# Performance work log

Measured on AMD Instinct MI355X. Metric: run time of the kernel, lower is better.

## Reference

```python
import jax, jax.numpy as jnp
import numpy as np

B, S, T, E, H, V = 32, 64, 64, 512, 512, 32000  # batch, src len, tgt len, embed, hidden(per dir), vocab


def _lstm_scan(xs, Wih, Whh, bih, bhh, h0, c0):
    # xs: [S, B, E]; PyTorch gate order i, f, g, o
    def step(carry, x):
        h, c = carry
        g = x @ Wih.T + bih + h @ Whh.T + bhh
        i, f, gg, o = jnp.split(g, 4, axis=-1)
        c = jax.nn.sigmoid(f) * c + jax.nn.sigmoid(i) * jnp.tanh(gg)
        h = jax.nn.sigmoid(o) * jnp.tanh(c)
        return (h, c), h
    (hT, cT), hs = jax.lax.scan(step, (h0, c0), xs)
    return hs, hT, cT


def setup_inputs() -> dict:
    key = jax.random.key(0)
    ks = jax.random.split(key, 20)
    p = lambda k, shape, s=0.05: (jax.random.normal(k, shape, jnp.float32) * s)
    inp = {
        "input_chunk": jax.random.randint(ks[0], (B, S), 0, V),
        "target_chunk": jax.random.randint(ks[1], (B, T), 0, V),
        "enc_emb": jax.random.uniform(ks[2], (V, E), jnp.float32, -0.1, 0.1),
        "dec_emb": jax.random.uniform(ks[3], (V, E), jnp.float32, -0.1, 0.1),
        # encoder bidirectional LSTM (1 layer)
        "Wih_f": p(ks[4], (4 * H, E)), "Whh_f": p(ks[5], (4 * H, H)),
        "bih_f": p(ks[6], (4 * H,)), "bhh_f": p(ks[7], (4 * H,)),
        "Wih_b": p(ks[8], (4 * H, E)), "Whh_b": p(ks[9], (4 * H, H)),
        "bih_b": p(ks[10], (4 * H,)), "bhh_b": p(ks[11], (4 * H,)),
        # decoder LSTMCell: input 2H+E, hidden 2H
        "Wih_d": p(ks[12], (8 * H, 2 * H + E)), "Whh_d": p(ks[13], (8 * H, 2 * H)),
        "bih_d": p(ks[14], (8 * H,)), "bhh_d": p(ks[15], (8 * H,)),
        # attention projection 2H -> 2H
        "Wa": p(ks[16], (2 * H, 2 * H)), "ba": p(ks[17], (2 * H,)),
        # output projection 2H -> V (bias initialized to 0 in the module)
        "Wout": p(ks[18], (V, 2 * H)), "bout": jnp.zeros((V,), jnp.float32),
    }
    return inp


def reference(input_chunk, target_chunk, enc_emb, dec_emb,
              Wih_f, Whh_f, bih_f, bhh_f, Wih_b, Whh_b, bih_b, bhh_b,
              Wih_d, Whh_d, bih_d, bhh_d, Wa, ba, Wout, bout):
    # ---- Encoder: bidirectional LSTM ----
    x = enc_emb[input_chunk]                 # [B, S, E]
    xs = jnp.transpose(x, (1, 0, 2))         # [S, B, E]
    h0 = jnp.zeros((B, H), x.dtype)
    c0 = jnp.zeros((B, H), x.dtype)
    hs_f, hT_f, cT_f = _lstm_scan(xs, Wih_f, Whh_f, bih_f, bhh_f, h0, c0)
    hs_b, hT_b, cT_b = _lstm_scan(xs[::-1], Wih_b, Whh_b, bih_b, bhh_b, h0, c0)
    hs_b = hs_b[::-1]
    all_hidden = jnp.concatenate([hs_f, hs_b], axis=-1)          # [S, B, 2H]
    all_hidden = jnp.transpose(all_hidden, (1, 0, 2))            # [B, S, 2H]
    dec_h = jnp.concatenate([hT_f, hT_b], axis=-1)               # [B, 2H]
    dec_c = jnp.concatenate([cT_f, cT_b], axis=-1)               # [B, 2H]

    # ---- Decoder: attention + LSTMCell loop (teacher forcing = 1.0, no dropout) ----
    A = all_hidden @ Wa.T + ba               # W_attention(all_hidden), constant across steps
    tgt_emb = dec_emb[target_chunk]          # [B, T, E]
    # feed at t=0 is zeros; afterwards the t-th target embedding
    feeds = jnp.concatenate([jnp.zeros((B, 1, E), tgt_emb.dtype), tgt_emb[:, :-1]], axis=1)
    feeds = jnp.transpose(feeds, (1, 0, 2))  # [T, B, E]

    def dstep(carry, feed):
        h, c = carry
        scores = jnp.einsum('bsd,bd->bs', A, h)                  # [B, S]
        attn = jax.nn.softmax(scores, axis=1)
        ctx = jnp.einsum('bs,bsd->bd', attn, all_hidden)         # [B, 2H]
        inp = jnp.concatenate([ctx, feed], axis=1)               # [B, 2H+E]
        g = inp @ Wih_d.T + bih_d + h @ Whh_d.T + bhh_d
        i, f, gg, o = jnp.split(g, 4, axis=-1)
        c = jax.nn.sigmoid(f) * c + jax.nn.sigmoid(i) * jnp.tanh(gg)
        h = jax.nn.sigmoid(o) * jnp.tanh(c)
        logits = h @ Wout.T + bout                               # [B, V]
        return (h, c), logits

    _, logits = jax.lax.scan(dstep, (dec_h, dec_c), feeds)       # [T, B, V]
    logits = jnp.transpose(logits, (1, 0, 2))                    # [B, T, V]
    outputs = jnp.argmax(logits, axis=-1)                        # [B, T]
    return logits, outputs
```

## Files before the change

kernel.cpp:

```cpp
#include <hip/hip_runtime.h>
#include <hip/hip_bf16.h>

#define BB 32
#define SS 64
#define TT 64
#define EE 512
#define HH 512
#define VV 32000

#define O_C0    0u
#define O_C1    32768u
#define O_HD    65536u
#define O_CD    98304u
#define O_PENC  131072u
#define O_PDEC  655360u
#define O_CTX   1179648u
#define O_ALLH  1212416u
#define O_AATT  3309568u
#define O_HDEC  5406720u
#define O_PACK  7503872u
#define O_DA1   7507968u
#define O_DA2   7540736u
#define O_W1    7573504u
#define WS_NEED 95830016ull

#define S_GXF   0u
#define S_GXB   4194304u
#define S_GFEED 8388608u
#define U_BASE  17000000u

typedef float f32x4 __attribute__((ext_vector_type(4)));
typedef _Float16 f16x8 __attribute__((ext_vector_type(8)));
typedef _Float16 f16x4 __attribute__((ext_vector_type(4)));

__device__ __forceinline__ float sigm_(float x){ return 1.0f/(1.0f + expf(-x)); }

__device__ __forceinline__ unsigned int fkey_(float f){
  unsigned int u = __float_as_uint(f);
  return (u & 0x80000000u) ? ~u : (u | 0x80000000u);
}

__device__ __forceinline__ int swz_(int row, int kb){
  return (row*64 + kb) ^ ((row & 7) << 4);
}

__global__ __launch_bounds__(256) void k_init(float* __restrict__ ws){
  int i = blockIdx.x*256 + threadIdx.x;
  if (i < 65536) ws[i] = 0.0f;
  if (i < 2048) ((unsigned long long*)(ws + O_PACK))[i] = 0ull;
}

__global__ __launch_bounds__(256) void k_cvtW(
    const float* __restrict__ Whh_f, const float* __restrict__ Whh_b,
    const float* __restrict__ Wih_d, const float* __restrict__ Whh_d,
    _Float16* __restrict__ dst)
{
  int g = blockIdx.x*256 + threadIdx.x;
  int idx = g*4;
  f32x4 v;
  if (idx < 1048576){
    v = *(const f32x4*)(Whh_f + idx);
  } else if (idx < 2097152){
    v = *(const f32x4*)(Whh_b + (idx - 1048576));
  } else {
    int j = idx - 2097152;
    int row = j >> 11, col = j & 2047;
    const float* src = (col < 1024) ? (Wih_d + (size_t)row*1536 + col)
                                    : (Whh_d + (size_t)row*1024 + (col - 1024));
    v = *(const f32x4*)src;
  }
  f16x4 h;
  #pragma unroll
  for (int c = 0; c < 4; ++c) h[c] = (_Float16)v[c];
  *(f16x4*)(dst + idx) = h;
}

__global__ __launch_bounds__(256) void k_cvtWout(
    const float* __restrict__ Wout, _Float16* __restrict__ W1)
{
  size_t i = ((size_t)blockIdx.x*256 + threadIdx.x)*8;
  f32x4 x0 = *(const f32x4*)(Wout + i);
  f32x4 x1 = *(const f32x4*)(Wout + i + 4);
  f16x4 h0, h1;
  #pragma unroll
  for (int c = 0; c < 4; ++c){ h0[c] = (_Float16)x0[c]; h1[c] = (_Float16)x1[c]; }
  *(f16x4*)(W1 + i)   = h0;
  *(f16x4*)(W1 + i+4) = h1;
}

template<int MODE>
__global__ __launch_bounds__(256) void k_gemm(
    const float* __restrict__ A, int lda,
    const int* __restrict__ chunk,
    const float* __restrict__ W, int ldW,
    const float* __restrict__ bias0, const float* __restrict__ bias1,
    float* __restrict__ C, int ldC, int K)
{
  __shared__ float As[16*68];
  __shared__ float Bs[16*68];
  int tid = threadIdx.x;
  int n0 = blockIdx.x*64, m0 = blockIdx.y*64;
  int tx = tid & 15, ty = tid >> 4;
  int lrow = tid >> 2, kq = tid & 3;

  const float* arp;
  if (MODE == 0) {
    arp = A + (size_t)(m0 + lrow)*lda;
  } else if (MODE == 1) {
    int m = m0 + lrow; int s = m >> 5, b = m & 31;
    arp = A + (size_t)chunk[b*SS + s]*EE;
  } else {
    int m = m0 + lrow; int t = m >> 5, b = m & 31;
    arp = (t == 0) ? nullptr : A + (size_t)chunk[b*TT + (t-1)]*EE;
  }
  const float* wrp = W + (size_t)(n0 + lrow)*ldW;

  float acc[4][4] = {};
  for (int k0 = 0; k0 < K; k0 += 16){
    float4 va = make_float4(0.f,0.f,0.f,0.f);
    if (MODE == 0) va = *(const float4*)&arp[k0 + kq*4];
    else if (arp)  va = *(const float4*)&arp[k0 + kq*4];
    float4 vw = *(const float4*)&wrp[k0 + kq*4];
    As[(kq*4+0)*68 + lrow] = va.x;
    As[(kq*4+1)*68 + lrow] = va.y;
    As[(kq*4+2)*68 + lrow] = va.z;
    As[(kq*4+3)*68 + lrow] = va.w;
    Bs[(kq*4+0)*68 + lrow] = vw.x;
    Bs[(kq*4+1)*68 + lrow] = vw.y;
    Bs[(kq*4+2)*68 + lrow] = vw.z;
    Bs[(kq*4+3)*68 + lrow] = vw.w;
    __syncthreads();
    #pragma unroll
    for (int kk = 0; kk < 16; ++kk){
      float4 a4 = *(const float4*)&As[kk*68 + ty*4];
      float4 b4 = *(const float4*)&Bs[kk*68 + tx*4];
      float av[4] = {a4.x,a4.y,a4.z,a4.w};
      float bv[4] = {b4.x,b4.y,b4.z,b4.w};
      #pragma unroll
      for (int i=0;i<4;++i)
        #pragma unroll
        for (int j=0;j<4;++j)
          acc[i][j] = fmaf(av[i], bv[j], acc[i][j]);
    }
    __syncthreads();
  }
  float bv[4];
  #pragma unroll
  for (int j = 0; j < 4; ++j){
    int n = n0 + tx*4 + j;
    float bb = 0.f;
    if (bias0) bb += bias0[n];
    if (bias1) bb += bias1[n];
    bv[j] = bb;
  }
  #pragma unroll
  for (int i = 0; i < 4; ++i){
    int m = m0 + ty*4 + i;
    float4 v = make_float4(acc[i][0]+bv[0], acc[i][1]+bv[1], acc[i][2]+bv[2], acc[i][3]+bv[3]);
    *(float4*)&C[(size_t)m*ldC + n0 + tx*4] = v;
  }
}

__global__ __launch_bounds__(256) void k_enc_step(
    const _Float16* __restrict__ wenc,
    float* __restrict__ ws, const float* __restrict__ oscr, int t)
{
  __shared__ float hl[128*36];
  __shared__ float Wt[32*132];
  int sub = blockIdx.x, kp = blockIdx.y, dir = blockIdx.z;
  int tid = threadIdx.x;
  int s = dir ? (63 - t) : t;
  int p = t & 1;
  const float* gx  = oscr + (dir ? S_GXB : S_GXF);
  const float* prd = ws + (p ? O_PDEC : O_PENC) + dir*262144u;
  const float* cin = ws + O_C0 + p*32768u + dir*16384u;
  float* cout = ws + O_C0 + (p^1)*32768u + dir*16384u;

  {
    int ug = tid & 31, bg = tid >> 5;
    int ul0 = ug*4;
    int u0 = kp*128 + ul0;
    #pragma unroll
    for (int j = 0; j < 4; ++j){
      int b = bg*4 + j;
      size_t gbase = (size_t)(s*32 + b)*2048u;
      f32x4 g0 = *(const f32x4*)&gx[gbase + u0];
      f32x4 g1 = *(const f32x4*)&gx[gbase + 512 + u0];
      f32x4 g2 = *(const f32x4*)&gx[gbase + 1024 + u0];
      f32x4 g3 = *(const f32x4*)&gx[gbase + 1536 + u0];
      if (t > 0){
        #pragma unroll
        for (int kq = 0; kq < 4; ++kq){
          const float* pp = prd + kq*65536u + (size_t)b*2048u;
          g0 += *(const f32x4*)&pp[u0];
          g1 += *(const f32x4*)&pp[512 + u0];
          g2 += *(const f32x4*)&pp[1024 + u0];
          g3 += *(const f32x4*)&pp[1536 + u0];
        }
      }
      f32x4 c = *(const f32x4*)&cin[b*512 + u0];
      f32x4 cn, hn;
      #pragma unroll
      for (int e = 0; e < 4; ++e){
        float cc = sigm_(g1[e])*c[e] + sigm_(g0[e])*tanhf(g2[e]);
        float hh = sigm_(g3[e])*tanhf(cc);
        cn[e] = cc; hn[e] = hh;
        hl[(ul0+e)*36 + b] = hh;
      }
      if (sub == 0){
        *(f32x4*)&cout[b*512 + u0] = cn;
        *(f32x4*)&ws[O_ALLH + (size_t)(b*64 + s)*1024u + dir*512 + u0] = hn;
      }
    }
  }
  __syncthreads();
  if (t == 63) return;

  const _Float16* W = wenc + dir*1048576u;
  float* P = ws + (p ? O_PENC : O_PDEC) + dir*262144u + kp*65536u;
  int rg2 = tid & 31, bg2 = tid >> 5;
  int wrow = tid & 127, whalf = tid >> 7;
  float acc[4][4] = {};
  for (int kt = 0; kt < 4; ++kt){
    #pragma unroll
    for (int i = 0; i < 4; ++i){
      int chunk = whalf*4 + i;
      int grow = sub*128 + wrow;
      f16x4 v = *(const f16x4*)&W[(size_t)grow*512 + kp*128 + kt*32 + chunk*4];
      Wt[(chunk*4+0)*132 + wrow] = (float)v[0];
      Wt[(chunk*4+1)*132 + wrow] = (float)v[1];
      Wt[(chunk*4+2)*132 + wrow] = (float)v[2];
      Wt[(chunk*4+3)*132 + wrow] = (float)v[3];
    }
    __syncthreads();
    #pragma unroll 8
    for (int kk = 0; kk < 32; ++kk){
      f32x4 wv = *(const f32x4*)&Wt[kk*132 + rg2*4];
      f32x4 hv = *(const f32x4*)&hl[(kt*32+kk)*36 + bg2*4];
      #pragma unroll
      for (int i = 0; i < 4; ++i)
        #pragma unroll
        for (int j = 0; j < 4; ++j)
          acc[i][j] = fmaf(wv[i], hv[j], acc[i][j]);
    }
    __syncthreads();
  }
  #pragma unroll
  for (int j = 0; j < 4; ++j){
    int b = bg2*4 + j;
    f32x4 v; v[0]=acc[0][j]; v[1]=acc[1][j]; v[2]=acc[2][j]; v[3]=acc[3][j];
    *(f32x4*)&P[(size_t)b*2048u + sub*128 + rg2*4] = v;
  }
}

__global__ __launch_bounds__(256) void k_concat(float* __restrict__ ws){
  int i = blockIdx.x*256 + threadIdx.x;
  int which = i >> 15;
  int idx = i & 32767;
  int b = idx >> 10, u = idx & 1023;
  int dir = (u >= 512);
  int uu = u & 511;
  float v;
  if (which == 0){
    int s = dir ? 0 : 63;
    v = ws[O_ALLH + (size_t)(b*64 + s)*1024u + u];
  } else {
    v = ws[O_C0 + dir*16384u + b*512 + uu];
  }
  ws[(which ? O_CD : O_HD) + b*1024 + u] = v;
}

__global__ __launch_bounds__(256) void k_dec_gemm(
    const _Float16* __restrict__ wdec, float* __restrict__ ws)
{
  __shared__ char lds[16384];
  int nb = blockIdx.x, kp = blockIdx.y;
  int tid = threadIdx.x;
  int lane = tid & 63, w = tid >> 6;
  int lr = lane & 15, lg = lane >> 4;
  const _Float16* A1g = (const _Float16*)(ws + O_DA1);
  const _Float16* A2g = (const _Float16*)(ws + O_DA2);

  int aslot = tid & 127;
  int isA2  = tid >> 7;
  int arow = aslot >> 2, aseg = aslot & 3;
  int wrow = tid >> 2, wseg = tid & 3;
  const _Float16* asrc = (isA2 ? A2g : A1g) + (size_t)arow*2048u + kp*512 + aseg*8;
  const _Float16* wsrc = wdec + (size_t)(nb*64 + wrow)*2048u + kp*512 + wseg*8;

  f32x4 accH[2], accM[2];
  #pragma unroll
  for (int i = 0; i < 2; ++i){ f32x4 z; z[0]=z[1]=z[2]=z[3]=0.f; accH[i]=z; accM[i]=z; }

  uint4 rA = *(const uint4*)(asrc);
  uint4 rW = *(const uint4*)(wsrc);

  for (int kt = 0; kt < 16; ++kt){
    int cur = kt & 1;
    char* base = lds + cur*8192;
    *(uint4*)(base + (isA2 ? 2048 : 0) + swz_(arow, aseg*16)) = rA;
    *(uint4*)(base + 4096 + swz_(wrow, wseg*16)) = rW;
    __syncthreads();
    if (kt < 15){
      rA = *(const uint4*)(asrc + (kt+1)*32);
      rW = *(const uint4*)(wsrc + (kt+1)*32);
    }
    char* A1t = base, *A2t = base + 2048, *Wt = base + 4096;
    f16x8 wf = *(const f16x8*)(Wt + swz_(w*16 + lr, lg*16));
    #pragma unroll
    for (int mf = 0; mf < 2; ++mf){
      f16x8 a1 = *(const f16x8*)(A1t + swz_(mf*16 + lr, lg*16));
      f16x8 a2 = *(const f16x8*)(A2t + swz_(mf*16 + lr, lg*16));
      accH[mf] = __builtin_amdgcn_mfma_f32_16x16x32_f16(a1, wf, accH[mf], 0, 0, 0);
      accM[mf] = __builtin_amdgcn_mfma_f32_16x16x32_f16(a2, wf, accM[mf], 0, 0, 0);
    }
    __syncthreads();
  }
  const float rs = 1.0f/2048.0f;
  float* P = ws + O_PDEC + (size_t)kp*131072u;
  #pragma unroll
  for (int mf = 0; mf < 2; ++mf)
    #pragma unroll
    for (int r = 0; r < 4; ++r){
      int b = mf*16 + lg*4 + r;
      int n = nb*64 + w*16 + lr;
      P[(size_t)b*4096u + n] = accH[mf][r] + accM[mf][r]*rs;
    }
}

__global__ __launch_bounds__(256) void k_attn(float* __restrict__ ws,
                                              const float* __restrict__ oscr, int t){
  __shared__ float hlq[1024];
  __shared__ float part[64][5];
  __shared__ float sc[64];
  __shared__ float atn[64];
  __shared__ float dsh;
  int b = blockIdx.x, tid = threadIdx.x;
  float* hd = ws + O_HD;
  float* cd = ws + O_CD;
  _Float16* DA1 = (_Float16*)(ws + O_DA1);
  _Float16* DA2 = (_Float16*)(ws + O_DA2);
  if (t > 0){
    const float* gfd = oscr + S_GFEED + (size_t)((t-1)*32 + b)*4096u;
    const float* pd = ws + O_PDEC;
    for (int u = tid; u < 1024; u += 256){
      float g0 = gfd[u], g1 = gfd[1024+u], g2 = gfd[2048+u], g3 = gfd[3072+u];
      #pragma unroll
      for (int kp = 0; kp < 4; ++kp){
        const float* p = pd + (size_t)kp*131072u + (size_t)b*4096u;
        g0 += p[u]; g1 += p[1024+u]; g2 += p[2048+u]; g3 += p[3072+u];
      }
      float c = cd[b*1024 + u];
      c = sigm_(g1)*c + sigm_(g0)*tanhf(g2);
      float h = sigm_(g3)*tanhf(c);
      cd[b*1024+u] = c; hd[b*1024+u] = h; hlq[u] = h;
      ws[O_HDEC + (size_t)(b*64 + (t-1))*1024u + u] = h;
      _Float16 hi = (_Float16)h;
      DA1[(size_t)b*2048u + 1024 + u] = hi;
      DA2[(size_t)b*2048u + 1024 + u] = (_Float16)((h - (float)hi)*2048.0f);
    }
  } else {
    for (int u = tid; u < 1024; u += 256){
      float h = hd[b*1024 + u];
      hlq[u] = h;
      _Float16 hi = (_Float16)h;
      DA1[(size_t)b*2048u + 1024 + u] = hi;
      DA2[(size_t)b*2048u + 1024 + u] = (_Float16)((h - (float)hi)*2048.0f);
    }
  }
  __syncthreads();
  {
    int s = tid >> 2, p = tid & 3;
    const float* Ar = ws + O_AATT + (size_t)(b*64 + s)*1024u + p*256;
    const float* hp = &hlq[p*256];
    float sum = 0.f;
    #pragma unroll 8
    for (int k4 = 0; k4 < 64; ++k4){
      float4 a = *(const float4*)&Ar[k4*4];
      float4 h4 = *(const float4*)&hp[k4*4];
      sum = fmaf(a.x,h4.x, fmaf(a.y,h4.y, fmaf(a.z,h4.z, fmaf(a.w,h4.w, sum))));
    }
    part[s][p] = sum;
  }
  __syncthreads();
  if (tid < 64) sc[tid] = part[tid][0] + part[tid][1] + part[tid][2] + part[tid][3];
  __syncthreads();
  if (tid < 64){
    float m = sc[0];
    #pragma unroll
    for (int i = 1; i < 64; ++i) m = fmaxf(m, sc[i]);
    atn[tid] = expf(sc[tid] - m);
  }
  __syncthreads();
  if (tid == 0){
    float d = 0.f;
    #pragma unroll
    for (int i = 0; i < 64; ++i) d += atn[i];
    dsh = 1.0f/d;
  }
  __syncthreads();
  {
    float rd = dsh;
    float ax=0.f, ay=0.f, az=0.f, aw=0.f;
    const float* ah = ws + O_ALLH + (size_t)(b*64)*1024u + tid*4;
    for (int s2 = 0; s2 < 64; ++s2){
      float a = atn[s2];
      float4 v = *(const float4*)&ah[(size_t)s2*1024u];
      ax = fmaf(a, v.x, ax); ay = fmaf(a, v.y, ay);
      az = fmaf(a, v.z, az); aw = fmaf(a, v.w, aw);
    }
    float o[4] = {ax*rd, ay*rd, az*rd, aw*rd};
    #pragma unroll
    for (int j = 0; j < 4; ++j){
      int u = tid*4 + j;
      _Float16 hi = (_Float16)o[j];
      DA1[(size_t)b*2048u + u] = hi;
      DA2[(size_t)b*2048u + u] = (_Float16)((o[j] - (float)hi)*2048.0f);
    }
  }
}

__global__ __launch_bounds__(256) void k_fin(float* __restrict__ ws,
                                             const float* __restrict__ oscr){
  int bid = blockIdx.x, tid = threadIdx.x;
  if ((bid & 3) == 3){
    int b = bid >> 2;
    const float* gfd = oscr + S_GFEED + (size_t)(63*32 + b)*4096u;
    const float* pd = ws + O_PDEC;
    for (int q = 0; q < 4; ++q){
      int u = q*256 + tid;
      float g0 = gfd[u], g1 = gfd[1024+u], g2 = gfd[2048+u], g3 = gfd[3072+u];
      #pragma unroll
      for (int kp = 0; kp < 4; ++kp){
        const float* p = pd + (size_t)kp*131072u + (size_t)b*4096u;
        g0 += p[u]; g1 += p[1024+u]; g2 += p[2048+u]; g3 += p[3072+u];
      }
      float c = ws[O_CD + b*1024 + u];
      c = sigm_(g1)*c + sigm_(g0)*tanhf(g2);
      float h = sigm_(g3)*tanhf(c);
      ws[O_HDEC + (size_t)(b*64 + 63)*1024u + u] = h;
    }
  }
  __syncthreads();
  const float* src = ws + O_HDEC;
  _Float16* A1 = (_Float16*)(ws + O_ALLH);
  _Float16* A2 = (_Float16*)(ws + O_AATT);
  for (int rep = 0; rep < 8; ++rep){
    int i = bid*16384 + (rep*256 + tid)*8;
    f32x4 x0 = *(const f32x4*)&src[i];
    f32x4 x1 = *(const f32x4*)&src[i+4];
    f16x4 h0, h1, l0, l1;
    #pragma unroll
    for (int c = 0; c < 4; ++c){
      _Float16 a = (_Float16)x0[c];
      h0[c] = a; l0[c] = (_Float16)((x0[c] - (float)a)*2048.0f);
      _Float16 bq = (_Float16)x1[c];
      h1[c] = bq; l1[c] = (_Float16)((x1[c] - (float)bq)*2048.0f);
    }
    *(f16x4*)&A1[i]   = h0;
    *(f16x4*)&A1[i+4] = h1;
    *(f16x4*)&A2[i]   = l0;
    *(f16x4*)&A2[i+4] = l1;
  }
}

__global__ __launch_bounds__(256) void k_logits(
    const _Float16* __restrict__ A1, const _Float16* __restrict__ A2,
    const _Float16* __restrict__ W1, const float* __restrict__ bout,
    float* __restrict__ out, unsigned long long* __restrict__ pk)
{
  __shared__ char lds[49152];
  int tid = threadIdx.x;
  int n0 = blockIdx.y*128, m0 = blockIdx.x*128;
  int lane = tid & 63, wave = tid >> 6;
  int wm = wave >> 1, wn = wave & 1;
  int lr = lane & 15, lg = lane >> 4;

  int s0 = tid*2, s1 = tid*2 + 1;
  int ar0 = s0 >> 2, as0 = s0 & 3;
  int ar1 = s1 >> 2, as1 = s1 & 3;
  const _Float16* a1p0 = A1 + (size_t)(m0 + ar0)*1024u + as0*8;
  const _Float16* a1p1 = A1 + (size_t)(m0 + ar1)*1024u + as1*8;
  const _Float16* a2p0 = A2 + (size_t)(m0 + ar0)*1024u + as0*8;
  const _Float16* a2p1 = A2 + (size_t)(m0 + ar1)*1024u + as1*8;
  const _Float16* wp0  = W1 + (size_t)(n0 + ar0)*1024u + as0*8;
  const _Float16* wp1  = W1 + (size_t)(n0 + ar1)*1024u + as1*8;

  f32x4 accH[4][4], accM[4][4];
  #pragma unroll
  for (int i = 0; i < 4; ++i)
    #pragma unroll
    for (int j = 0; j < 4; ++j){
      f32x4 z; z[0]=z[1]=z[2]=z[3]=0.f;
      accH[i][j] = z; accM[i][j] = z;
    }

  uint4 r10, r11, r20, r21, rw0, rw1;
  r10 = *(const uint4*)a1p0; r11 = *(const uint4*)a1p1;
  r20 = *(const uint4*)a2p0; r21 = *(const uint4*)a2p1;
  rw0 = *(const uint4*)wp0;  rw1 = *(const uint4*)wp1;

  for (int kt = 0; kt < 32; ++kt){
    int cur = kt & 1;
    char* base = lds + cur*24576;
    char* A1t = base, *A2t = base + 8192, *Wt = base + 16384;
    *(uint4*)(A1t + swz_(ar0, as0*16)) = r10;
    *(uint4*)(A1t + swz_(ar1, as1*16)) = r11;
    *(uint4*)(A2t + swz_(ar0, as0*16)) = r20;
    *(uint4*)(A2t + swz_(ar1, as1*16)) = r21;
    *(uint4*)(Wt  + swz_(ar0, as0*16)) = rw0;
    *(uint4*)(Wt  + swz_(ar1, as1*16)) = rw1;
    __syncthreads();
    if (kt < 31){
      int ko = (kt+1)*32;
      r10 = *(const uint4*)(a1p0 + ko); r11 = *(const uint4*)(a1p1 + ko);
      r20 = *(const uint4*)(a2p0 + ko); r21 = *(const uint4*)(a2p1 + ko);
      rw0 = *(const uint4*)(wp0 + ko);  rw1 = *(const uint4*)(wp1 + ko);
    }
    f16x8 wf[4];
    #pragma unroll
    for (int nf = 0; nf < 4; ++nf)
      wf[nf] = *(const f16x8*)(Wt + swz_(wn*64 + nf*16 + lr, lg*16));
    #pragma unroll
    for (int mf = 0; mf < 4; ++mf){
      int ad = swz_(wm*64 + mf*16 + lr, lg*16);
      f16x8 a1f = *(const f16x8*)(A1t + ad);
      f16x8 a2f = *(const f16x8*)(A2t + ad);
      #pragma unroll
      for (int nf = 0; nf < 4; ++nf){
        accH[mf][nf] = __builtin_amdgcn_mfma_f32_16x16x32_f16(a1f, wf[nf], accH[mf][nf], 0, 0, 0);
        accM[mf][nf] = __builtin_amdgcn_mfma_f32_16x16x32_f16(a2f, wf[nf], accM[mf][nf], 0, 0, 0);
      }
    }
    __syncthreads();
  }

  const float rs = 1.0f/2048.0f;
  float bb[4];
  #pragma unroll
  for (int nf = 0; nf < 4; ++nf) bb[nf] = bout[n0 + wn*64 + nf*16 + lr];
  #pragma unroll
  for (int mf = 0; mf < 4; ++mf){
    #pragma unroll
    for (int r = 0; r < 4; ++r){
      int m = m0 + wm*64 + mf*16 + lg*4 + r;
      unsigned long long bk = 0ull;
      #pragma unroll
      for (int nf = 0; nf < 4; ++nf){
        int n = n0 + wn*64 + nf*16 + lr;
        float val = accH[mf][nf][r] + accM[mf][nf][r]*rs + bb[nf];
        __builtin_nontemporal_store(val, &out[(size_t)m*VV + n]);
        unsigned long long p = ((unsigned long long)fkey_(val) << 32) | (unsigned int)(~(unsigned int)n);
        if (p > bk) bk = p;
      }
      #pragma unroll
      for (int off = 1; off < 16; off <<= 1){
        unsigned long long o = __shfl_xor(bk, off, 64);
        if (o > bk) bk = o;
      }
      if (lr == 0) atomicMax(&pk[m], bk);
    }
  }
}

__global__ __launch_bounds__(512) void k_logits_fb(
    const _Float16* __restrict__ A1, const _Float16* __restrict__ A2,
    const float* __restrict__ Wout, const float* __restrict__ bout,
    float* __restrict__ out, unsigned long long* __restrict__ pk)
{
  __shared__ char lds[49152];
  char* A1t = lds;
  char* A2t = lds + 8192;
  char* W1t = lds + 16384;
  char* W2t = lds + 32768;
  int tid = threadIdx.x;
  int n0 = blockIdx.x*256;
  int lane = tid & 63, wave = tid >> 6;
  int wm = wave >> 2, wn = wave & 3;
  int lr = lane & 15, lg = lane >> 4;

  int arow = tid >> 2, aseg = tid & 3;
  int wrow = tid >> 1, wseg = tid & 1;
  const float* wp = Wout + (size_t)(n0 + wrow)*1024u + wseg*16;

  float bb[4];
  #pragma unroll
  for (int nf = 0; nf < 4; ++nf) bb[nf] = bout[n0 + wn*64 + nf*16 + lr];
  const float rs = 1.0f/2048.0f;

  for (int mi = 0; mi < 4; ++mi){
    int m0 = (blockIdx.y*4 + mi)*128;
    const _Float16* a1p = A1 + (size_t)(m0 + arow)*1024u + aseg*8;
    const _Float16* a2p = A2 + (size_t)(m0 + arow)*1024u + aseg*8;

    f32x4 accH[4][4], accM[4][4];
    #pragma unroll
    for (int i = 0; i < 4; ++i)
      #pragma unroll
      for (int j = 0; j < 4; ++j){
        f32x4 z; z[0]=z[1]=z[2]=z[3]=0.f;
        accH[i][j] = z; accM[i][j] = z;
      }

    for (int k0 = 0; k0 < 1024; k0 += 32){
      uint4 av1 = *(const uint4*)(a1p + k0);
      uint4 av2 = *(const uint4*)(a2p + k0);
      f32x4 wv[4];
      #pragma unroll
      for (int i = 0; i < 4; ++i) wv[i] = *(const f32x4*)(wp + k0 + i*4);
      __syncthreads();
      *(uint4*)(A1t + swz_(arow, aseg*16)) = av1;
      *(uint4*)(A2t + swz_(arow, aseg*16)) = av2;
      f16x8 hi[2], lo[2];
      #pragma unroll
      for (int i = 0; i < 2; ++i)
        #pragma unroll
        for (int c = 0; c < 8; ++c){
          float x = wv[i*2 + (c>>2)][c&3];
          _Float16 h = (_Float16)x;
          hi[i][c] = h;
          lo[i][c] = (_Float16)((x - (float)h)*2048.0f);
        }
      *(f16x8*)(W1t + swz_(wrow, wseg*32 +  0)) = hi[0];
      *(f16x8*)(W1t + swz_(wrow, wseg*32 + 16)) = hi[1];
      *(f16x8*)(W2t + swz_(wrow, wseg*32 +  0)) = lo[0];
      *(f16x8*)(W2t + swz_(wrow, wseg*32 + 16)) = lo[1];
      __syncthreads();
      f16x8 w1f[4], w2f[4];
      #pragma unroll
      for (int nf = 0; nf < 4; ++nf){
        int ad = swz_(wn*64 + nf*16 + lr, lg*16);
        w1f[nf] = *(const f16x8*)(W1t + ad);
        w2f[nf] = *(const f16x8*)(W2t + ad);
      }
      #pragma unroll
      for (int mf = 0; mf < 4; ++mf){
        int ad = swz_(wm*64 + mf*16 + lr, lg*16);
        f16x8 a1f = *(const f16x8*)(A1t + ad);
        f16x8 a2f = *(const f16x8*)(A2t + ad);
        #pragma unroll
        for (int nf = 0; nf < 4; ++nf){
          accH[mf][nf] = __builtin_amdgcn_mfma_f32_16x16x32_f16(a1f, w1f[nf], accH[mf][nf], 0, 0, 0);
          accM[mf][nf] = __builtin_amdgcn_mfma_f32_16x16x32_f16(a1f, w2f[nf], accM[mf][nf], 0, 0, 0);
          accM[mf][nf] = __builtin_amdgcn_mfma_f32_16x16x32_f16(a2f, w1f[nf], accM[mf][nf], 0, 0, 0);
        }
      }
    }

    #pragma unroll
    for (int mf = 0; mf < 4; ++mf){
      #pragma unroll
      for (int r = 0; r < 4; ++r){
        int m = m0 + wm*64 + mf*16 + lg*4 + r;
        unsigned long long bk = 0ull;
        #pragma unroll
        for (int nf = 0; nf < 4; ++nf){
          int n = n0 + wn*64 + nf*16 + lr;
          float val = accH[mf][nf][r] + accM[mf][nf][r]*rs + bb[nf];
          __builtin_nontemporal_store(val, &out[(size_t)m*VV + n]);
          unsigned long long p = ((unsigned long long)fkey_(val) << 32) | (unsigned int)(~(unsigned int)n);
          if (p > bk) bk = p;
        }
        #pragma unroll
        for (int off = 1; off < 16; off <<= 1){
          unsigned long long o = __shfl_xor(bk, off, 64);
          if (o > bk) bk = o;
        }
        if (lr == 0) atomicMax(&pk[m], bk);
      }
    }
  }
}

__global__ __launch_bounds__(256) void k_argmax(
    const unsigned long long* __restrict__ pk, float* __restrict__ out)
{
  int i = blockIdx.x*256 + threadIdx.x;
  if (i < 2048){
    unsigned int low = (unsigned int)(pk[i] & 0xFFFFFFFFull);
    unsigned int col = ~low;
    out[(size_t)BB*TT*VV + i] = (float)col;
  }
}

extern "C" void kernel_launch(void* const* d_in, const int* in_sizes, int n_in,
                              void* d_out, int out_size, void* d_ws, size_t ws_size,
                              hipStream_t stream)
{
  const int*   input_chunk  = (const int*)d_in[0];
  const int*   target_chunk = (const int*)d_in[1];
  const float* enc_emb = (const float*)d_in[2];
  const float* dec_emb = (const float*)d_in[3];
  const float* Wih_f = (const float*)d_in[4];
  const float* Whh_f = (const float*)d_in[5];
  const float* bih_f = (const float*)d_in[6];
  const float* bhh_f = (const float*)d_in[7];
  const float* Wih_b = (const float*)d_in[8];
  const float* Whh_b = (const float*)d_in[9];
  const float* bih_b = (const float*)d_in[10];
  const float* bhh_b = (const float*)d_in[11];
  const float* Wih_d = (const float*)d_in[12];
  const float* Whh_d = (const float*)d_in[13];
  const float* bih_d = (const float*)d_in[14];
  const float* bhh_d = (const float*)d_in[15];
  const float* Wa   = (const float*)d_in[16];
  const float* ba   = (const float*)d_in[17];
  const float* Wout = (const float*)d_in[18];
  const float* bout = (const float*)d_in[19];
  float* ws = (float*)d_ws;
  float* out = (float*)d_out;
  float* oscr = (float*)d_out;
  _Float16* wf16 = (_Float16*)(oscr + U_BASE);
  bool bigws = (ws_size >= WS_NEED);

  k_init<<<256, 256, 0, stream>>>(ws);
  k_cvtW<<<10240, 256, 0, stream>>>(Whh_f, Whh_b, Wih_d, Whh_d, wf16);
  if (bigws)
    k_cvtWout<<<16000, 256, 0, stream>>>(Wout, (_Float16*)(ws + O_W1));

  k_gemm<1><<<dim3(32,32), 256, 0, stream>>>(enc_emb, 512, input_chunk, Wih_f, 512, bih_f, bhh_f, oscr + S_GXF, 2048, 512);
  k_gemm<1><<<dim3(32,32), 256, 0, stream>>>(enc_emb, 512, input_chunk, Wih_b, 512, bih_b, bhh_b, oscr + S_GXB, 2048, 512);
  k_gemm<2><<<dim3(64,32), 256, 0, stream>>>(dec_emb, 512, target_chunk, Wih_d + 1024, 1536, bih_d, bhh_d, oscr + S_GFEED, 4096, 512);

  for (int t = 0; t < 64; ++t){
    k_enc_step<<<dim3(16,4,2), 256, 0, stream>>>(wf16, ws, oscr, t);
  }

  k_concat<<<256, 256, 0, stream>>>(ws);
  k_gemm<0><<<dim3(16,32), 256, 0, stream>>>(ws + O_ALLH, 1024, nullptr, Wa, 1024, ba, nullptr, ws + O_AATT, 1024, 1024);

  const _Float16* wdec = wf16 + 2097152u;
  for (int t = 0; t < 64; ++t){
    k_attn<<<32, 256, 0, stream>>>(ws, oscr, t);
    k_dec_gemm<<<dim3(64,4), 256, 0, stream>>>(wdec, ws);
  }
  k_fin<<<128, 256, 0, stream>>>(ws, oscr);

  if (bigws){
    k_logits<<<dim3(16,250), 256, 0, stream>>>(
        (const _Float16*)(ws + O_ALLH), (const _Float16*)(ws + O_AATT),
        (const _Float16*)(ws + O_W1), bout, out, (unsigned long long*)(ws + O_PACK));
  } else {
    k_logits_fb<<<dim3(125,4), 512, 0, stream>>>(
        (const _Float16*)(ws + O_ALLH), (const _Float16*)(ws + O_AATT),
        Wout, bout, out, (unsigned long long*)(ws + O_PACK));
  }
  k_argmax<<<8, 256, 0, stream>>>((const unsigned long long*)(ws + O_PACK), out);
}
```

Measured before the change: 3.500 ms.

## Replace FP32 input-projection GEMMs with split-fp16 MFMA kernel

The three input-projection GEMMs (encoder forward/backward and decoder feed) move from a scalar FP32 tiled kernel to a new MFMA kernel. Activations are split into high and scaled-low fp16 parts to keep accuracy, while the weights are converted to fp16 in the extended conversion kernel. Global loads are double-buffered through swizzled LDS. The aim is to use matrix cores for these GEMMs, at the cost of extra weight conversion work and some precision loss from fp16 weights.

```diff
diff --git a/kernel.cpp b/kernel.cpp
--- a/kernel.cpp
+++ b/kernel.cpp
@@ -28,6 +28,10 @@
 #define S_GXB   4194304u
 #define S_GFEED 8388608u
 #define U_BASE  17000000u
+#define U_WIHF  10485760u
+#define U_WIHB  11534336u
+#define U_WFEED 12582912u
+#define U_TOTAL 14680064u
 
 typedef float f32x4 __attribute__((ext_vector_type(4)));
 typedef _Float16 f16x8 __attribute__((ext_vector_type(8)));
@@ -53,21 +57,31 @@
 __global__ __launch_bounds__(256) void k_cvtW(
     const float* __restrict__ Whh_f, const float* __restrict__ Whh_b,
     const float* __restrict__ Wih_d, const float* __restrict__ Whh_d,
+    const float* __restrict__ Wih_f, const float* __restrict__ Wih_b,
     _Float16* __restrict__ dst)
 {
   int g = blockIdx.x*256 + threadIdx.x;
-  int idx = g*4;
+  unsigned idx = (unsigned)g*4u;
+  if (idx >= U_TOTAL) return;
   f32x4 v;
-  if (idx < 1048576){
+  if (idx < 1048576u){
     v = *(const f32x4*)(Whh_f + idx);
-  } else if (idx < 2097152){
-    v = *(const f32x4*)(Whh_b + (idx - 1048576));
+  } else if (idx < 2097152u){
+    v = *(const f32x4*)(Whh_b + (idx - 1048576u));
+  } else if (idx < U_WIHF){
+    unsigned j = idx - 2097152u;
+    unsigned row = j >> 11, col = j & 2047u;
+    const float* src = (col < 1024u) ? (Wih_d + (size_t)row*1536 + col)
+                                     : (Whh_d + (size_t)row*1024 + (col - 1024u));
+    v = *(const f32x4*)src;
+  } else if (idx < U_WIHB){
+    v = *(const f32x4*)(Wih_f + (idx - U_WIHF));
+  } else if (idx < U_WFEED){
+    v = *(const f32x4*)(Wih_b + (idx - U_WIHB));
   } else {
-    int j = idx - 2097152;
-    int row = j >> 11, col = j & 2047;
-    const float* src = (col < 1024) ? (Wih_d + (size_t)row*1536 + col)
-                                    : (Whh_d + (size_t)row*1024 + (col - 1024));
-    v = *(const f32x4*)src;
+    unsigned j = idx - U_WFEED;
+    unsigned row = j >> 9, col = j & 511u;
+    v = *(const f32x4*)(Wih_d + (size_t)row*1536 + 1024 + col);
   }
   f16x4 h;
   #pragma unroll
@@ -158,6 +172,125 @@
     int m = m0 + ty*4 + i;
     float4 v = make_float4(acc[i][0]+bv[0], acc[i][1]+bv[1], acc[i][2]+bv[2], acc[i][3]+bv[3]);
     *(float4*)&C[(size_t)m*ldC + n0 + tx*4] = v;
+  }
+}
+
+template<int MODE>
+__global__ __launch_bounds__(256) void k_proj(
+    const float* __restrict__ emb, const int* __restrict__ chunk,
+    const _Float16* __restrict__ Wh,
+    const float* __restrict__ bias0, const float* __restrict__ bias1,
+    float* __restrict__ C, int ldC)
+{
+  __shared__ char lds[49152];
+  int tid = threadIdx.x;
+  int n0 = blockIdx.x*128, m0 = blockIdx.y*128;
+  int lane = tid & 63, wave = tid >> 6;
+  int wm = wave >> 1, wn = wave & 1;
+  int lr = lane & 15, lg = lane >> 4;
+
+  int s0 = tid*2, s1 = tid*2 + 1;
+  int ar0 = s0 >> 2, as0 = s0 & 3;
+  int ar1 = s1 >> 2, as1 = s1 & 3;
+
+  const float* arp0; const float* arp1;
+  {
+    int m = m0 + ar0;
+    if (MODE == 1){ int s = m >> 5, b = m & 31; arp0 = emb + (size_t)chunk[b*SS + s]*EE + as0*8; }
+    else { int tt = m >> 5, b = m & 31; arp0 = tt ? (emb + (size_t)chunk[b*TT + (tt-1)]*EE + as0*8) : nullptr; }
+    m = m0 + ar1;
+    if (MODE == 1){ int s = m >> 5, b = m & 31; arp1 = emb + (size_t)chunk[b*SS + s]*EE + as1*8; }
+    else { int tt = m >> 5, b = m & 31; arp1 = tt ? (emb + (size_t)chunk[b*TT + (tt-1)]*EE + as1*8) : nullptr; }
+  }
+  const _Float16* wp0 = Wh + (size_t)(n0 + ar0)*512u + as0*8;
+  const _Float16* wp1 = Wh + (size_t)(n0 + ar1)*512u + as1*8;
+
+  f32x4 accH[4][4], accM[4][4];
+  #pragma unroll
+  for (int i = 0; i < 4; ++i)
+    #pragma unroll
+    for (int j = 0; j < 4; ++j){
+      f32x4 z; z[0]=z[1]=z[2]=z[3]=0.f;
+      accH[i][j] = z; accM[i][j] = z;
+    }
+
+  f32x4 zz; zz[0]=zz[1]=zz[2]=zz[3]=0.f;
+  f32x4 a0a, a0b, a1a, a1b;
+  uint4 rw0, rw1;
+  a0a = arp0 ? *(const f32x4*)(arp0)     : zz;
+  a0b = arp0 ? *(const f32x4*)(arp0 + 4) : zz;
+  a1a = arp1 ? *(const f32x4*)(arp1)     : zz;
+  a1b = arp1 ? *(const f32x4*)(arp1 + 4) : zz;
+  rw0 = *(const uint4*)wp0;
+  rw1 = *(const uint4*)wp1;
+
+  for (int kt = 0; kt < 16; ++kt){
+    char* base = lds + (kt & 1)*24576;
+    char* A1t = base, *A2t = base + 8192, *Wt = base + 16384;
+    f16x8 h0, l0, h1, l1;
+    #pragma unroll
+    for (int c = 0; c < 4; ++c){
+      float x = a0a[c]; _Float16 hh = (_Float16)x;
+      h0[c] = hh; l0[c] = (_Float16)((x - (float)hh)*2048.0f);
+      x = a0b[c]; hh = (_Float16)x;
+      h0[4+c] = hh; l0[4+c] = (_Float16)((x - (float)hh)*2048.0f);
+      x = a1a[c]; hh = (_Float16)x;
+      h1[c] = hh; l1[c] = (_Float16)((x - (float)hh)*2048.0f);
+      x = a1b[c]; hh = (_Float16)x;
+      h1[4+c] = hh; l1[4+c] = (_Float16)((x - (float)hh)*2048.0f);
+    }
+    *(f16x8*)(A1t + swz_(ar0, as0*16)) = h0;
+    *(f16x8*)(A2t + swz_(ar0, as0*16)) = l0;
+    *(f16x8*)(A1t + swz_(ar1, as1*16)) = h1;
+    *(f16x8*)(A2t + swz_(ar1, as1*16)) = l1;
+    *(uint4*)(Wt + swz_(ar0, as0*16)) = rw0;
+    *(uint4*)(Wt + swz_(ar1, as1*16)) = rw1;
+    __syncthreads();
+    if (kt < 15){
+      int ko = (kt+1)*32;
+      a0a = arp0 ? *(const f32x4*)(arp0 + ko)     : zz;
+      a0b = arp0 ? *(const f32x4*)(arp0 + ko + 4) : zz;
+      a1a = arp1 ? *(const f32x4*)(arp1 + ko)     : zz;
+      a1b = arp1 ? *(const f32x4*)(arp1 + ko + 4) : zz;
+      rw0 = *(const uint4*)(wp0 + ko);
+      rw1 = *(const uint4*)(wp1 + ko);
+    }
+    f16x8 wf[4];
+    #pragma unroll
+    for (int nf = 0; nf < 4; ++nf)
+      wf[nf] = *(const f16x8*)(Wt + swz_(wn*64 + nf*16 + lr, lg*16));
+    #pragma unroll
+    for (int mf = 0; mf < 4; ++mf){
+      int ad = swz_(wm*64 + mf*16 + lr, lg*16);
+      f16x8 a1f = *(const f16x8*)(A1t + ad);
+      f16x8 a2f = *(const f16x8*)(A2t + ad);
+      #pragma unroll
+      for (int nf = 0; nf < 4; ++nf){
+        accH[mf][nf] = __builtin_amdgcn_mfma_f32_16x16x32_f16(a1f, wf[nf], accH[mf][nf], 0, 0, 0);
+        accM[mf][nf] = __builtin_amdgcn_mfma_f32_16x16x32_f16(a2f, wf[nf], accM[mf][nf], 0, 0, 0);
+      }
+    }
+    __syncthreads();
+  }
+
+  const float rs = 1.0f/2048.0f;
+  float bb[4];
+  #pragma unroll
+  for (int nf = 0; nf < 4; ++nf){
+    int n = n0 + wn*64 + nf*16 + lr;
+    bb[nf] = bias0[n] + bias1[n];
+  }
+  #pragma unroll
+  for (int mf = 0; mf < 4; ++mf){
+    #pragma unroll
+    for (int r = 0; r < 4; ++r){
+      int m = m0 + wm*64 + mf*16 + lg*4 + r;
+      #pragma unroll
+      for (int nf = 0; nf < 4; ++nf){
+        int n = n0 + wn*64 + nf*16 + lr;
+        C[(size_t)m*ldC + n] = accH[mf][nf][r] + accM[mf][nf][r]*rs + bb[nf];
+      }
+    }
   }
 }
 
@@ -714,13 +847,13 @@
   bool bigws = (ws_size >= WS_NEED);
 
   k_init<<<256, 256, 0, stream>>>(ws);
-  k_cvtW<<<10240, 256, 0, stream>>>(Whh_f, Whh_b, Wih_d, Whh_d, wf16);
+  k_cvtW<<<14336, 256, 0, stream>>>(Whh_f, Whh_b, Wih_d, Whh_d, Wih_f, Wih_b, wf16);
   if (bigws)
     k_cvtWout<<<16000, 256, 0, stream>>>(Wout, (_Float16*)(ws + O_W1));
 
-  k_gemm<1><<<dim3(32,32), 256, 0, stream>>>(enc_emb, 512, input_chunk, Wih_f, 512, bih_f, bhh_f, oscr + S_GXF, 2048, 512);
-  k_gemm<1><<<dim3(32,32), 256, 0, stream>>>(enc_emb, 512, input_chunk, Wih_b, 512, bih_b, bhh_b, oscr + S_GXB, 2048, 512);
-  k_gemm<2><<<dim3(64,32), 256, 0, stream>>>(dec_emb, 512, target_chunk, Wih_d + 1024, 1536, bih_d, bhh_d, oscr + S_GFEED, 4096, 512);
+  k_proj<1><<<dim3(16,16), 256, 0, stream>>>(enc_emb, input_chunk, wf16 + U_WIHF, bih_f, bhh_f, oscr + S_GXF, 2048);
+  k_proj<1><<<dim3(16,16), 256, 0, stream>>>(enc_emb, input_chunk, wf16 + U_WIHB, bih_b, bhh_b, oscr + S_GXB, 2048);
+  k_proj<2><<<dim3(32,16), 256, 0, stream>>>(dec_emb, target_chunk, wf16 + U_WFEED, bih_d, bhh_d, oscr + S_GFEED, 4096);
 
   for (int t = 0; t < 64; ++t){
     k_enc_step<<<dim3(16,4,2), 256, 0, stream>>>(wf16, ws, oscr, t);
```

Result: faster. 3.315 ms (-5.3%).
